# Optimization experiments

Measured on AMD Instinct MI355X. Metric: run time of the kernel, lower is better.

Reference implementation:

```python
import jax, jax.numpy as jnp
import numpy as np

N_NODES = 100000
N_EDGES = 1600000
H_IN = 128
H_OUT = 128
ELU_ALPHA = 0.1


def setup_inputs() -> dict:
    key = jax.random.key(0)
    k = jax.random.split(key, 6)
    x = jax.random.normal(k[0], (N_NODES, H_IN), dtype=jnp.float32)
    edge_index = jax.random.randint(k[1], (2, N_EDGES), 0, N_NODES, dtype=jnp.int64)
    s = 1.0 / np.sqrt(H_IN)
    W_conv = jax.random.uniform(k[2], (H_IN, H_OUT), jnp.float32, -s, s)
    b_conv = jnp.zeros((H_OUT,), jnp.float32)
    W_skip = jax.random.uniform(k[3], (H_IN, H_OUT), jnp.float32, -s, s)
    b_skip = jax.random.uniform(k[4], (H_OUT,), jnp.float32, -s, s)
    return {"x": x, "edge_index": edge_index, "W_conv": W_conv,
            "b_conv": b_conv, "W_skip": W_skip, "b_skip": b_skip}


def reference(x, edge_index, W_conv, b_conv, W_skip, b_skip):
    # GCNConv(improved=True): add self-loops with weight 2.0, symmetric norm.
    N = x.shape[0]
    src, dst = edge_index[0], edge_index[1]
    # degree = incoming edge weights (1.0 each) + 2.0 self-loop weight
    deg = jnp.zeros((N,), x.dtype).at[dst].add(1.0) + 2.0
    dinv = jax.lax.rsqrt(deg)                     # deg >= 2 always
    norm = dinv[src] * dinv[dst]                  # [E]
    h = x @ W_conv                                # [N, H_OUT]
    # scatter-add of normalized messages over real edges
    agg = jax.ops.segment_sum(norm[:, None] * h[src], dst, num_segments=N)
    # self-loop contribution: weight 2 * dinv[i]^2
    agg = agg + (2.0 * dinv * dinv)[:, None] * h
    out = agg + b_conv + x @ W_skip + b_skip
    # Dropout(p=0.1) in eval mode = identity; ELU(alpha=0.1)
    return jnp.where(out > 0, out, ELU_ALPHA * (jnp.exp(out) - 1.0))
```

## Files before the change

### kernel.cpp

```cpp
#include <hip/hip_runtime.h>
#include <hip/hip_bf16.h>
#include <hip/hip_fp16.h>

#define H 128
#define BW 128
#define BSH 7
#define NB 256

typedef __attribute__((ext_vector_type(8))) short short8;
typedef __attribute__((ext_vector_type(4))) float f32x4;

__device__ inline unsigned short f2bf(float f) {
    union { float f; unsigned int u; } v; v.f = f;
    unsigned int r = (v.u + 0x7fffu + ((v.u >> 16) & 1u)) >> 16;
    return (unsigned short)r;
}
__device__ inline float bf2f(unsigned short h) {
    union { unsigned int u; float f; } v; v.u = ((unsigned int)h) << 16;
    return v.f;
}

__global__ __launch_bounds__(256) void quant_hist_kernel(const float* __restrict__ x,
                                                         const float* __restrict__ Wc,
                                                         const float* __restrict__ Ws,
                                                         const int* __restrict__ ei,
                                                         uint* __restrict__ xq,
                                                         float* __restrict__ invs,
                                                         short8* __restrict__ wp,
                                                         int* __restrict__ counts,
                                                         int N, int E, int nbu,
                                                         int chunk, int qb) {
    __shared__ int h[1024];
    if (blockIdx.x >= qb) {
        const int b = blockIdx.x - qb;
        for (int i = threadIdx.x; i < nbu; i += 256) h[i] = 0;
        __syncthreads();
        const int lo = b * chunk;
        const int hi = min(E, lo + chunk);
        for (int e = lo + threadIdx.x; e < hi; e += 256)
            atomicAdd(&h[ei[E + e] >> BSH], 1);
        __syncthreads();
        for (int i = threadIdx.x; i < nbu; i += 256) counts[b * nbu + i] = h[i];
        return;
    }
    int node = blockIdx.x * 8 + (threadIdx.x >> 5);
    if (node < N) {
        int l32 = threadIdx.x & 31;
        float4 v = ((const float4*)x)[node * 32 + l32];
        float m = fmaxf(fmaxf(fabsf(v.x), fabsf(v.y)), fmaxf(fabsf(v.z), fabsf(v.w)));
        #pragma unroll
        for (int mk = 1; mk < 32; mk <<= 1) m = fmaxf(m, __shfl_xor(m, mk));
        m = fmaxf(m, 1e-30f);
        float s = 127.0f / m;
        int q0 = min(255, max(0, (int)rintf(v.x * s) + 128));
        int q1 = min(255, max(0, (int)rintf(v.y * s) + 128));
        int q2 = min(255, max(0, (int)rintf(v.z * s) + 128));
        int q3 = min(255, max(0, (int)rintf(v.w * s) + 128));
        xq[node * 32 + l32] = (uint)q0 | ((uint)q1 << 8) | ((uint)q2 << 16) | ((uint)q3 << 24);
        if (l32 == 0) invs[node] = m / 127.0f;
    }
    if (blockIdx.x < 8) {
        int t = blockIdx.x * 256 + threadIdx.x;
        int lane = t & 63;
        int nt = (t >> 6) & 7;
        int ks = t >> 9;
        int kbase = ks * 32 + (lane >> 4) * 8;
        int col = nt * 16 + (lane & 15);
        short8 whc, whs, wls;
        #pragma unroll
        for (int j = 0; j < 8; ++j) {
            float wc = Wc[(kbase + j) * H + col];
            float ws = Ws[(kbase + j) * H + col];
            unsigned short hc = f2bf(wc);
            unsigned short hs = f2bf(ws);
            whc[j] = (short)hc;
            whs[j] = (short)hs;
            wls[j] = (short)f2bf(ws - bf2f(hs));
        }
        int base = (ks * 8 + nt) * 64 + lane;
        wp[base] = whc;
        wp[2048 + base] = whs;
        wp[4096 + base] = wls;
    }
}

__global__ __launch_bounds__(NB) void p2_scan(const int* __restrict__ counts,
                                              int* __restrict__ scanned,
                                              int* __restrict__ btot, int nbu) {
    __shared__ int s[NB];
    const int k = blockIdx.x, t = threadIdx.x;
    int v = counts[t * nbu + k];
    s[t] = v;
    __syncthreads();
    for (int off = 1; off < NB; off <<= 1) {
        int a = (t >= off) ? s[t - off] : 0;
        __syncthreads();
        s[t] += a;
        __syncthreads();
    }
    scanned[t * nbu + k] = s[t] - v;
    if (t == NB - 1) btot[k] = s[t];
}

__global__ __launch_bounds__(256) void p5_scatter(const int* __restrict__ ei,
                                                  const int* __restrict__ btot,
                                                  const int* __restrict__ scanned,
                                                  int* __restrict__ tmp,
                                                  int* __restrict__ cstart,
                                                  int E, int nbu, int chunk) {
    __shared__ int sc[1024];
    __shared__ int part[256];
    __shared__ int lb[1024];
    const int t = threadIdx.x;
    const int b = blockIdx.x;
    const int base = t * 4;
    int v0 = (base + 0 < nbu) ? btot[base + 0] : 0;
    int v1 = (base + 1 < nbu) ? btot[base + 1] : 0;
    int v2 = (base + 2 < nbu) ? btot[base + 2] : 0;
    int v3 = (base + 3 < nbu) ? btot[base + 3] : 0;
    int s1 = v0 + v1, s2 = s1 + v2, s3 = s2 + v3;
    part[t] = s3;
    __syncthreads();
    for (int off = 1; off < 256; off <<= 1) {
        int a = (t >= off) ? part[t - off] : 0;
        __syncthreads();
        part[t] += a;
        __syncthreads();
    }
    int add = (t > 0) ? part[t - 1] : 0;
    sc[base + 0] = add;
    sc[base + 1] = add + v0;
    sc[base + 2] = add + s1;
    sc[base + 3] = add + s2;
    __syncthreads();
    if (b == 0) {
        for (int k = t; k < nbu; k += 256) cstart[k] = sc[k];
        if (t == 0) cstart[nbu] = E;
    }
    for (int k = t; k < nbu; k += 256) lb[k] = sc[k] + scanned[b * nbu + k];
    __syncthreads();
    const int lo = b * chunk;
    const int hi = min(E, lo + chunk);
    for (int e = lo + t; e < hi; e += 256) {
        int s = ei[e], d = ei[E + e];
        int slot = atomicAdd(&lb[d >> BSH], 1);
        tmp[slot] = ((d & (BW - 1)) << 17) | s;
    }
}

__global__ __launch_bounds__(256) void csra_kernel(const int* __restrict__ tmp,
                                                   const int* __restrict__ cstart,
                                                   const float* __restrict__ invs,
                                                   int* __restrict__ rstart,
                                                   float* __restrict__ dinv,
                                                   float* __restrict__ ainv,
                                                   float* __restrict__ selfw,
                                                   int N, int E) {
    __shared__ int ldeg[BW];
    __shared__ int lscan[BW];
    const int b = blockIdx.x;
    const int nstart = b << BSH;
    const int estart = cstart[b];
    const int eend = cstart[b + 1];
    const int t = threadIdx.x;

    if (t < BW) ldeg[t] = 0;
    __syncthreads();
    for (int i = estart + t; i < eend; i += 256)
        atomicAdd(&ldeg[(tmp[i] >> 17) & (BW - 1)], 1);
    __syncthreads();
    if (t < BW) lscan[t] = ldeg[t];
    __syncthreads();
    #pragma unroll
    for (int off = 1; off < BW; off <<= 1) {
        int a = 0;
        if (t < BW && t >= off) a = lscan[t - off];
        __syncthreads();
        if (t < BW) lscan[t] += a;
        __syncthreads();
    }
    if (t < BW) {
        int excl = lscan[t] - ldeg[t];
        int n = nstart + t;
        if (n < N) {
            float iv = invs[n];
            float dv = rsqrtf((float)ldeg[t] + 2.0f);
            rstart[n] = estart + excl;
            dinv[n] = dv;
            ainv[n] = dv * iv;
            selfw[n] = 2.0f * dv * dv * iv;
        }
    }
    if (b == 0 && t == 0) rstart[N] = E;
}

__global__ __launch_bounds__(256) void csrb_kernel(const int* __restrict__ tmp,
                                                   const int* __restrict__ cstart,
                                                   const int* __restrict__ rstart,
                                                   const float* __restrict__ dinv,
                                                   const float* __restrict__ ainv,
                                                   int* __restrict__ entries,
                                                   unsigned short* __restrict__ wgt,
                                                   int N, int E) {
    __shared__ int lcur[BW];
    __shared__ float ldv[BW];
    const int b = blockIdx.x;
    const int nstart = b << BSH;
    const int t = threadIdx.x;
    if (t < BW) {
        int n = nstart + t;
        lcur[t] = (n < N) ? rstart[n] : 0;
        ldv[t] = (n < N) ? dinv[n] : 0.f;
    }
    __syncthreads();
    const int estart = cstart[b];
    const int eend = cstart[b + 1];
    for (int i = estart + t; i < eend; i += 256) {
        int v = tmp[i];
        int ld = (v >> 17) & (BW - 1);
        int src = v & 0x1FFFF;
        float w = ainv[src] * ldv[ld];
        int slot = atomicAdd(&lcur[ld], 1);
        entries[slot] = src;
        wgt[slot] = __half_as_ushort(__float2half(w));
    }
}

__global__ __launch_bounds__(256) void agg_kernel(const int* __restrict__ entries,
                                                  const unsigned short* __restrict__ wgt,
                                                  const int* __restrict__ rstart,
                                                  const float* __restrict__ selfw,
                                                  const uint* __restrict__ xq,
                                                  unsigned short* __restrict__ z, int N) {
    int node = blockIdx.x * 16 + (threadIdx.x >> 4);
    if (node >= N) return;
    const int l16 = threadIdx.x & 15;
    const uint2* x2 = (const uint2*)xq;

    int start = rstart[node];
    int end = rstart[node + 1];
    float sw = selfw[node];
    uint2 qs = x2[node * 16 + l16];

    float a0 = 0.f, a1 = 0.f, a2 = 0.f, a3 = 0.f;
    float a4 = 0.f, a5 = 0.f, a6 = 0.f, a7 = 0.f;
    float sumw = 0.f;

    for (int c = start; c < end; c += 16) {
        int rem = end - c;
        int src = 0;
        float w = 0.f;
        if (l16 < rem) {
            src = entries[c + l16];
            w = __half2float(__ushort_as_half(wgt[c + l16]));
        }
        #pragma unroll 4
        for (int j = 0; j < 16; ++j) {
            int ss = __shfl(src, j, 16);
            float wv = __shfl(w, j, 16);
            if (wv != 0.f) {
                uint2 q = x2[ss * 16 + l16];
                sumw += wv;
                a0 += wv * (float)(q.x & 0xffu);
                a1 += wv * (float)((q.x >> 8) & 0xffu);
                a2 += wv * (float)((q.x >> 16) & 0xffu);
                a3 += wv * (float)(q.x >> 24);
                a4 += wv * (float)(q.y & 0xffu);
                a5 += wv * (float)((q.y >> 8) & 0xffu);
                a6 += wv * (float)((q.y >> 16) & 0xffu);
                a7 += wv * (float)(q.y >> 24);
            }
        }
    }

    sumw += sw;
    a0 += sw * (float)(qs.x & 0xffu);
    a1 += sw * (float)((qs.x >> 8) & 0xffu);
    a2 += sw * (float)((qs.x >> 16) & 0xffu);
    a3 += sw * (float)(qs.x >> 24);
    a4 += sw * (float)(qs.y & 0xffu);
    a5 += sw * (float)((qs.y >> 8) & 0xffu);
    a6 += sw * (float)((qs.y >> 16) & 0xffu);
    a7 += sw * (float)(qs.y >> 24);

    float off = 128.f * sumw;
    uint4 o;
    o.x = (uint)f2bf(a0 - off) | ((uint)f2bf(a1 - off) << 16);
    o.y = (uint)f2bf(a2 - off) | ((uint)f2bf(a3 - off) << 16);
    o.z = (uint)f2bf(a4 - off) | ((uint)f2bf(a5 - off) << 16);
    o.w = (uint)f2bf(a6 - off) | ((uint)f2bf(a7 - off) << 16);
    ((uint4*)z)[node * 16 + l16] = o;
}

__global__ __launch_bounds__(256) void gemm_kernel(const unsigned short* __restrict__ zb,
                                                   const float* __restrict__ x,
                                                   const short8* __restrict__ wp,
                                                   const float* __restrict__ bc,
                                                   const float* __restrict__ bsk,
                                                   float* __restrict__ out, int N) {
    __shared__ short8 bsm[1536];
    const int tid = threadIdx.x;
    const int lane = tid & 63;
    const int wave = tid >> 6;
    const int m = lane & 15;
    const int quad = lane >> 4;
    const int row = blockIdx.x * 64 + wave * 16 + m;
    const bool rowok = row < N;

    f32x4 acc[8];
    #pragma unroll
    for (int i = 0; i < 8; ++i) acc[i] = (f32x4){0.f, 0.f, 0.f, 0.f};

    #pragma unroll
    for (int ks = 0; ks < 4; ++ks) {
        const int k0 = ks * 32 + quad * 8;
        short8 za = {0, 0, 0, 0, 0, 0, 0, 0};
        short8 xa_h = {0, 0, 0, 0, 0, 0, 0, 0};
        short8 xa_l = {0, 0, 0, 0, 0, 0, 0, 0};
        if (rowok) {
            za = ((const short8*)zb)[(row * H + k0) >> 3];
            float4 a = *(const float4*)&x[row * H + k0];
            float4 b = *(const float4*)&x[row * H + k0 + 4];
            float xv[8] = {a.x, a.y, a.z, a.w, b.x, b.y, b.z, b.w};
            #pragma unroll
            for (int j = 0; j < 8; ++j) {
                unsigned short h = f2bf(xv[j]);
                xa_h[j] = (short)h;
                xa_l[j] = (short)f2bf(xv[j] - bf2f(h));
            }
        }
        __syncthreads();
        #pragma unroll
        for (int p = 0; p < 3; ++p) {
            bsm[p * 512 + tid]       = wp[p * 2048 + ks * 512 + tid];
            bsm[p * 512 + 256 + tid] = wp[p * 2048 + ks * 512 + 256 + tid];
        }
        __syncthreads();
        #pragma unroll
        for (int nt = 0; nt < 8; ++nt) {
            short8 bch = bsm[nt * 64 + lane];
            short8 bsh = bsm[512 + nt * 64 + lane];
            short8 bsl = bsm[1024 + nt * 64 + lane];
            acc[nt] = __builtin_amdgcn_mfma_f32_16x16x32_bf16(za, bch, acc[nt], 0, 0, 0);
            acc[nt] = __builtin_amdgcn_mfma_f32_16x16x32_bf16(xa_h, bsh, acc[nt], 0, 0, 0);
            acc[nt] = __builtin_amdgcn_mfma_f32_16x16x32_bf16(xa_l, bsh, acc[nt], 0, 0, 0);
            acc[nt] = __builtin_amdgcn_mfma_f32_16x16x32_bf16(xa_h, bsl, acc[nt], 0, 0, 0);
        }
    }

    const int orow_base = blockIdx.x * 64 + wave * 16 + quad * 4;
    #pragma unroll
    for (int nt = 0; nt < 8; ++nt) {
        int col = nt * 16 + m;
        float bias = bc[col] + bsk[col];
        #pragma unroll
        for (int r = 0; r < 4; ++r) {
            int orow = orow_base + r;
            if (orow < N) {
                float v = acc[nt][r] + bias;
                v = v > 0.f ? v : 0.1f * (__expf(v) - 1.f);
                out[orow * H + col] = v;
            }
        }
    }
}

extern "C" void kernel_launch(void* const* d_in, const int* in_sizes, int n_in,
                              void* d_out, int out_size, void* d_ws, size_t ws_size,
                              hipStream_t stream) {
    const float* x   = (const float*)d_in[0];
    const int*   ei  = (const int*)d_in[1];
    const float* Wc  = (const float*)d_in[2];
    const float* bc  = (const float*)d_in[3];
    const float* Wsk = (const float*)d_in[4];
    const float* bsk = (const float*)d_in[5];
    float* out = (float*)d_out;

    const int N = in_sizes[0] / H;
    const int E = in_sizes[1] / 2;
    const int nbu = (N + BW - 1) / BW;
    const int chunk = (E + NB - 1) / NB;
    const int qb = (N + 7) / 8;

    char* w = (char*)d_ws;
    short8*         wp      = (short8*)w;
    int*            rstart  = (int*)(w + 131072);
    float*          selfw   = (float*)(w + 589824);
    int*            entries = (int*)(w + 1048576);
    unsigned short* wgt     = (unsigned short*)(w + 7471104);
    uint*           xq      = (uint*)(w + 10747904);
    unsigned short* z       = (unsigned short*)(w + 23592960);
    float*          invs    = (float*)(w + 23592960);
    float*          dinv    = (float*)(w + 23992960);
    float*          ainv    = (float*)(w + 24392960);
    int*            cstart  = (int*)(w + 24792960);
    int*            btot    = (int*)(w + 24796160);
    int*            counts  = (int*)(w + 24799360);
    int*            scanned = (int*)(w + 25600128);
    int*            tmp     = (int*)(w + 26400896);

    quant_hist_kernel<<<qb + NB, 256, 0, stream>>>(x, Wc, Wsk, ei, xq, invs, wp,
                                                   counts, N, E, nbu, chunk, qb);

    p2_scan<<<nbu, NB, 0, stream>>>(counts, scanned, btot, nbu);
    p5_scatter<<<NB, 256, 0, stream>>>(ei, btot, scanned, tmp, cstart, E, nbu, chunk);
    csra_kernel<<<nbu, 256, 0, stream>>>(tmp, cstart, invs, rstart, dinv, ainv, selfw, N, E);
    csrb_kernel<<<nbu, 256, 0, stream>>>(tmp, cstart, rstart, dinv, ainv, entries, wgt, N, E);

    agg_kernel<<<(N + 15) / 16, 256, 0, stream>>>(entries, wgt, rstart, selfw, xq, z, N);

    gemm_kernel<<<(N + 63) / 64, 256, 0, stream>>>(z, x, wp, bc, bsk, out, N);
}
```

Before: 256.4 us.

## Build CSR with global per-node degree atomics instead of two-level bucket sort

Replaces the bucketed counting sort (per-block LDS histograms, cross-block scan, bucket scatter, then two per-bucket CSR passes) with per-node global atomic degree counts, a scan to get row starts, and one scatter pass that uses per-node global atomic cursors. This removes the intermediate tmp array and two full passes over the edges. In exchange it adds about 3.2M global atomics on random addresses plus a zero-init kernel, where the old code used LDS atomics. Edge order within each row is no longer deterministic, so fp accumulation order can vary between runs.

After: 370.7 us. +44.6%, slower.

```diff
diff --git a/kernel.cpp b/kernel.cpp
--- a/kernel.cpp
+++ b/kernel.cpp
@@ -20,27 +20,26 @@
     return v.f;
 }
 
-__global__ __launch_bounds__(256) void quant_hist_kernel(const float* __restrict__ x,
-                                                         const float* __restrict__ Wc,
-                                                         const float* __restrict__ Ws,
-                                                         const int* __restrict__ ei,
-                                                         uint* __restrict__ xq,
-                                                         float* __restrict__ invs,
-                                                         short8* __restrict__ wp,
-                                                         int* __restrict__ counts,
-                                                         int N, int E, int nbu,
-                                                         int chunk, int qb) {
-    __shared__ int h[1024];
+__global__ __launch_bounds__(256) void zero_kernel(int* __restrict__ p, int n) {
+    int i = blockIdx.x * 256 + threadIdx.x;
+    if (i < n) p[i] = 0;
+}
+
+__global__ __launch_bounds__(256) void quant_deg_kernel(const float* __restrict__ x,
+                                                        const float* __restrict__ Wc,
+                                                        const float* __restrict__ Ws,
+                                                        const int* __restrict__ ei,
+                                                        uint* __restrict__ xq,
+                                                        float* __restrict__ invs,
+                                                        short8* __restrict__ wp,
+                                                        int* __restrict__ deg,
+                                                        int N, int E, int chunk, int qb) {
     if (blockIdx.x >= qb) {
         const int b = blockIdx.x - qb;
-        for (int i = threadIdx.x; i < nbu; i += 256) h[i] = 0;
-        __syncthreads();
         const int lo = b * chunk;
         const int hi = min(E, lo + chunk);
         for (int e = lo + threadIdx.x; e < hi; e += 256)
-            atomicAdd(&h[ei[E + e] >> BSH], 1);
-        __syncthreads();
-        for (int i = threadIdx.x; i < nbu; i += 256) counts[b * nbu + i] = h[i];
+            atomicAdd(&deg[ei[E + e]], 1);
         return;
     }
     int node = blockIdx.x * 8 + (threadIdx.x >> 5);
@@ -84,35 +83,46 @@
     }
 }
 
-__global__ __launch_bounds__(NB) void p2_scan(const int* __restrict__ counts,
-                                              int* __restrict__ scanned,
-                                              int* __restrict__ btot, int nbu) {
-    __shared__ int s[NB];
-    const int k = blockIdx.x, t = threadIdx.x;
-    int v = counts[t * nbu + k];
-    s[t] = v;
+__global__ __launch_bounds__(BW) void metrics_kernel(const int* __restrict__ deg,
+                                                     const float* __restrict__ invs,
+                                                     float* __restrict__ dinv,
+                                                     float* __restrict__ ainv,
+                                                     float* __restrict__ selfw,
+                                                     int* __restrict__ lofs,
+                                                     int* __restrict__ btot, int N) {
+    __shared__ int s[BW];
+    const int b = blockIdx.x, t = threadIdx.x;
+    const int n = (b << BSH) + t;
+    int d = (n < N) ? deg[n] : 0;
+    s[t] = d;
     __syncthreads();
-    for (int off = 1; off < NB; off <<= 1) {
+    #pragma unroll
+    for (int off = 1; off < BW; off <<= 1) {
         int a = (t >= off) ? s[t - off] : 0;
         __syncthreads();
         s[t] += a;
         __syncthreads();
     }
-    scanned[t * nbu + k] = s[t] - v;
-    if (t == NB - 1) btot[k] = s[t];
-}
-
-__global__ __launch_bounds__(256) void p5_scatter(const int* __restrict__ ei,
-                                                  const int* __restrict__ btot,
-                                                  const int* __restrict__ scanned,
-                                                  int* __restrict__ tmp,
-                                                  int* __restrict__ cstart,
-                                                  int E, int nbu, int chunk) {
+    if (n < N) {
+        lofs[n] = s[t] - d;
+        float iv = invs[n];
+        float dv = rsqrtf((float)d + 2.0f);
+        dinv[n] = dv;
+        ainv[n] = dv * iv;
+        selfw[n] = 2.0f * dv * dv * iv;
+    }
+    if (t == BW - 1) btot[b] = s[t];
+}
+
+__global__ __launch_bounds__(256) void rstart_kernel(const int* __restrict__ btot,
+                                                     const int* __restrict__ lofs,
+                                                     const float* __restrict__ dinv,
+                                                     int* __restrict__ rstart,
+                                                     int2* __restrict__ pk,
+                                                     int N, int E, int nbu) {
     __shared__ int sc[1024];
     __shared__ int part[256];
-    __shared__ int lb[1024];
-    const int t = threadIdx.x;
-    const int b = blockIdx.x;
+    const int t = threadIdx.x, b = blockIdx.x;
     const int base = t * 4;
     int v0 = (base + 0 < nbu) ? btot[base + 0] : 0;
     int v1 = (base + 1 < nbu) ? btot[base + 1] : 0;
@@ -133,95 +143,33 @@
     sc[base + 2] = add + s1;
     sc[base + 3] = add + s2;
     __syncthreads();
-    if (b == 0) {
-        for (int k = t; k < nbu; k += 256) cstart[k] = sc[k];
-        if (t == 0) cstart[nbu] = E;
-    }
-    for (int k = t; k < nbu; k += 256) lb[k] = sc[k] + scanned[b * nbu + k];
-    __syncthreads();
-    const int lo = b * chunk;
+    const int cs = sc[b];
+    if (t < BW) {
+        int n = (b << BSH) + t;
+        if (n < N) {
+            int r = cs + lofs[n];
+            rstart[n] = r;
+            pk[n] = make_int2(r, __float_as_int(dinv[n]));
+        }
+    }
+    if (b == 0 && t == 0) rstart[N] = E;
+}
+
+__global__ __launch_bounds__(256) void scatter_kernel(const int* __restrict__ ei,
+                                                      const int2* __restrict__ pk,
+                                                      const float* __restrict__ ainv,
+                                                      int* __restrict__ cnt,
+                                                      int* __restrict__ entries,
+                                                      unsigned short* __restrict__ wgt,
+                                                      int E, int chunk) {
+    const int lo = blockIdx.x * chunk;
     const int hi = min(E, lo + chunk);
-    for (int e = lo + t; e < hi; e += 256) {
+    for (int e = lo + threadIdx.x; e < hi; e += 256) {
         int s = ei[e], d = ei[E + e];
-        int slot = atomicAdd(&lb[d >> BSH], 1);
-        tmp[slot] = ((d & (BW - 1)) << 17) | s;
-    }
-}
-
-__global__ __launch_bounds__(256) void csra_kernel(const int* __restrict__ tmp,
-                                                   const int* __restrict__ cstart,
-                                                   const float* __restrict__ invs,
-                                                   int* __restrict__ rstart,
-                                                   float* __restrict__ dinv,
-                                                   float* __restrict__ ainv,
-                                                   float* __restrict__ selfw,
-                                                   int N, int E) {
-    __shared__ int ldeg[BW];
-    __shared__ int lscan[BW];
-    const int b = blockIdx.x;
-    const int nstart = b << BSH;
-    const int estart = cstart[b];
-    const int eend = cstart[b + 1];
-    const int t = threadIdx.x;
-
-    if (t < BW) ldeg[t] = 0;
-    __syncthreads();
-    for (int i = estart + t; i < eend; i += 256)
-        atomicAdd(&ldeg[(tmp[i] >> 17) & (BW - 1)], 1);
-    __syncthreads();
-    if (t < BW) lscan[t] = ldeg[t];
-    __syncthreads();
-    #pragma unroll
-    for (int off = 1; off < BW; off <<= 1) {
-        int a = 0;
-        if (t < BW && t >= off) a = lscan[t - off];
-        __syncthreads();
-        if (t < BW) lscan[t] += a;
-        __syncthreads();
-    }
-    if (t < BW) {
-        int excl = lscan[t] - ldeg[t];
-        int n = nstart + t;
-        if (n < N) {
-            float iv = invs[n];
-            float dv = rsqrtf((float)ldeg[t] + 2.0f);
-            rstart[n] = estart + excl;
-            dinv[n] = dv;
-            ainv[n] = dv * iv;
-            selfw[n] = 2.0f * dv * dv * iv;
-        }
-    }
-    if (b == 0 && t == 0) rstart[N] = E;
-}
-
-__global__ __launch_bounds__(256) void csrb_kernel(const int* __restrict__ tmp,
-                                                   const int* __restrict__ cstart,
-                                                   const int* __restrict__ rstart,
-                                                   const float* __restrict__ dinv,
-                                                   const float* __restrict__ ainv,
-                                                   int* __restrict__ entries,
-                                                   unsigned short* __restrict__ wgt,
-                                                   int N, int E) {
-    __shared__ int lcur[BW];
-    __shared__ float ldv[BW];
-    const int b = blockIdx.x;
-    const int nstart = b << BSH;
-    const int t = threadIdx.x;
-    if (t < BW) {
-        int n = nstart + t;
-        lcur[t] = (n < N) ? rstart[n] : 0;
-        ldv[t] = (n < N) ? dinv[n] : 0.f;
-    }
-    __syncthreads();
-    const int estart = cstart[b];
-    const int eend = cstart[b + 1];
-    for (int i = estart + t; i < eend; i += 256) {
-        int v = tmp[i];
-        int ld = (v >> 17) & (BW - 1);
-        int src = v & 0x1FFFF;
-        float w = ainv[src] * ldv[ld];
-        int slot = atomicAdd(&lcur[ld], 1);
-        entries[slot] = src;
+        int2 p = pk[d];
+        float w = ainv[s] * __int_as_float(p.y);
+        int slot = p.x + atomicAdd(&cnt[d], 1);
+        entries[slot] = s;
         wgt[slot] = __half_as_ushort(__float2half(w));
     }
 }
@@ -393,19 +341,22 @@
     float*          invs    = (float*)(w + 23592960);
     float*          dinv    = (float*)(w + 23992960);
     float*          ainv    = (float*)(w + 24392960);
-    int*            cstart  = (int*)(w + 24792960);
-    int*            btot    = (int*)(w + 24796160);
-    int*            counts  = (int*)(w + 24799360);
-    int*            scanned = (int*)(w + 25600128);
-    int*            tmp     = (int*)(w + 26400896);
-
-    quant_hist_kernel<<<qb + NB, 256, 0, stream>>>(x, Wc, Wsk, ei, xq, invs, wp,
-                                                   counts, N, E, nbu, chunk, qb);
-
-    p2_scan<<<nbu, NB, 0, stream>>>(counts, scanned, btot, nbu);
-    p5_scatter<<<NB, 256, 0, stream>>>(ei, btot, scanned, tmp, cstart, E, nbu, chunk);
-    csra_kernel<<<nbu, 256, 0, stream>>>(tmp, cstart, invs, rstart, dinv, ainv, selfw, N, E);
-    csrb_kernel<<<nbu, 256, 0, stream>>>(tmp, cstart, rstart, dinv, ainv, entries, wgt, N, E);
+    int*            lofs    = (int*)(w + 24792960);
+    int*            btot    = (int*)(w + 25192960);
+    int*            deg     = (int*)(w + 25197056);
+    int*            cnt     = (int*)(w + 25597056);
+    int2*           pk      = (int2*)(w + 25997056);
+
+    zero_kernel<<<(2 * N + 255) / 256, 256, 0, stream>>>(deg, 2 * N);
+
+    quant_deg_kernel<<<qb + NB, 256, 0, stream>>>(x, Wc, Wsk, ei, xq, invs, wp,
+                                                  deg, N, E, chunk, qb);
+
+    metrics_kernel<<<nbu, BW, 0, stream>>>(deg, invs, dinv, ainv, selfw, lofs, btot, N);
+
+    rstart_kernel<<<nbu, 256, 0, stream>>>(btot, lofs, dinv, rstart, pk, N, E, nbu);
+
+    scatter_kernel<<<NB, 256, 0, stream>>>(ei, pk, ainv, cnt, entries, wgt, E, chunk);
 
     agg_kernel<<<(N + 15) / 16, 256, 0, stream>>>(entries, wgt, rstart, selfw, xq, z, N);
 
```

## Compute per-node degrees via global atomics in histogram pass, drop csra pass

Applied to the files above, without the earlier changes.

The histogram pass now also counts per-node in-degree with global atomics into a zeroed array. A new node_kernel derives row starts, dinv, ainv and self weights from those degrees plus the bucket totals, so the separate csra pass that re-read the bucketed edge buffer is removed. The exchange is a zeroing launch and 1.6M global atomics added to the histogram pass, against one fewer pass over the temporary edge array.

Result: slower. 333.5 us (+30.1%).

```diff
diff --git a/kernel.cpp b/kernel.cpp
--- a/kernel.cpp
+++ b/kernel.cpp
@@ -18,6 +18,11 @@
 __device__ inline float bf2f(unsigned short h) {
     union { unsigned int u; float f; } v; v.u = ((unsigned int)h) << 16;
     return v.f;
+}
+
+__global__ __launch_bounds__(256) void zero_kernel(int* __restrict__ p, int n) {
+    int i = blockIdx.x * 256 + threadIdx.x;
+    if (i < n) p[i] = 0;
 }
 
 __global__ __launch_bounds__(256) void quant_hist_kernel(const float* __restrict__ x,
@@ -28,6 +33,7 @@
                                                          float* __restrict__ invs,
                                                          short8* __restrict__ wp,
                                                          int* __restrict__ counts,
+                                                         int* __restrict__ deg,
                                                          int N, int E, int nbu,
                                                          int chunk, int qb) {
     __shared__ int h[1024];
@@ -37,8 +43,11 @@
         __syncthreads();
         const int lo = b * chunk;
         const int hi = min(E, lo + chunk);
-        for (int e = lo + threadIdx.x; e < hi; e += 256)
-            atomicAdd(&h[ei[E + e] >> BSH], 1);
+        for (int e = lo + threadIdx.x; e < hi; e += 256) {
+            int d = ei[E + e];
+            atomicAdd(&h[d >> BSH], 1);
+            atomicAdd(&deg[d], 1);
+        }
         __syncthreads();
         for (int i = threadIdx.x; i < nbu; i += 256) counts[b * nbu + i] = h[i];
         return;
@@ -100,6 +109,61 @@
     }
     scanned[t * nbu + k] = s[t] - v;
     if (t == NB - 1) btot[k] = s[t];
+}
+
+__global__ __launch_bounds__(256) void node_kernel(const int* __restrict__ deg,
+                                                   const float* __restrict__ invs,
+                                                   const int* __restrict__ btot,
+                                                   int* __restrict__ rstart,
+                                                   float* __restrict__ dinv,
+                                                   float* __restrict__ ainv,
+                                                   float* __restrict__ selfw,
+                                                   int N, int E, int nbu) {
+    __shared__ int sc[1024];
+    __shared__ int part[256];
+    __shared__ int s[BW];
+    const int t = threadIdx.x, b = blockIdx.x;
+    const int base = t * 4;
+    int v0 = (base + 0 < nbu) ? btot[base + 0] : 0;
+    int v1 = (base + 1 < nbu) ? btot[base + 1] : 0;
+    int v2 = (base + 2 < nbu) ? btot[base + 2] : 0;
+    int v3 = (base + 3 < nbu) ? btot[base + 3] : 0;
+    int s1 = v0 + v1, s2 = s1 + v2, s3 = s2 + v3;
+    part[t] = s3;
+    const int n = (b << BSH) + t;
+    int d = 0;
+    if (t < BW) { d = (n < N) ? deg[n] : 0; s[t] = d; }
+    __syncthreads();
+    for (int off = 1; off < 256; off <<= 1) {
+        int a = (t >= off) ? part[t - off] : 0;
+        __syncthreads();
+        part[t] += a;
+        __syncthreads();
+    }
+    int add = (t > 0) ? part[t - 1] : 0;
+    sc[base + 0] = add;
+    sc[base + 1] = add + v0;
+    sc[base + 2] = add + s1;
+    sc[base + 3] = add + s2;
+    #pragma unroll
+    for (int off = 1; off < BW; off <<= 1) {
+        int a = 0;
+        if (t < BW && t >= off) a = s[t - off];
+        __syncthreads();
+        if (t < BW) s[t] += a;
+        __syncthreads();
+    }
+    const int cs = sc[b];
+    if (t < BW && n < N) {
+        int excl = s[t] - d;
+        rstart[n] = cs + excl;
+        float iv = invs[n];
+        float dv = rsqrtf((float)d + 2.0f);
+        dinv[n] = dv;
+        ainv[n] = dv * iv;
+        selfw[n] = 2.0f * dv * dv * iv;
+    }
+    if (b == 0 && t == 0) rstart[N] = E;
 }
 
 __global__ __launch_bounds__(256) void p5_scatter(const int* __restrict__ ei,
@@ -148,52 +212,6 @@
     }
 }
 
-__global__ __launch_bounds__(256) void csra_kernel(const int* __restrict__ tmp,
-                                                   const int* __restrict__ cstart,
-                                                   const float* __restrict__ invs,
-                                                   int* __restrict__ rstart,
-                                                   float* __restrict__ dinv,
-                                                   float* __restrict__ ainv,
-                                                   float* __restrict__ selfw,
-                                                   int N, int E) {
-    __shared__ int ldeg[BW];
-    __shared__ int lscan[BW];
-    const int b = blockIdx.x;
-    const int nstart = b << BSH;
-    const int estart = cstart[b];
-    const int eend = cstart[b + 1];
-    const int t = threadIdx.x;
-
-    if (t < BW) ldeg[t] = 0;
-    __syncthreads();
-    for (int i = estart + t; i < eend; i += 256)
-        atomicAdd(&ldeg[(tmp[i] >> 17) & (BW - 1)], 1);
-    __syncthreads();
-    if (t < BW) lscan[t] = ldeg[t];
-    __syncthreads();
-    #pragma unroll
-    for (int off = 1; off < BW; off <<= 1) {
-        int a = 0;
-        if (t < BW && t >= off) a = lscan[t - off];
-        __syncthreads();
-        if (t < BW) lscan[t] += a;
-        __syncthreads();
-    }
-    if (t < BW) {
-        int excl = lscan[t] - ldeg[t];
-        int n = nstart + t;
-        if (n < N) {
-            float iv = invs[n];
-            float dv = rsqrtf((float)ldeg[t] + 2.0f);
-            rstart[n] = estart + excl;
-            dinv[n] = dv;
-            ainv[n] = dv * iv;
-            selfw[n] = 2.0f * dv * dv * iv;
-        }
-    }
-    if (b == 0 && t == 0) rstart[N] = E;
-}
-
 __global__ __launch_bounds__(256) void csrb_kernel(const int* __restrict__ tmp,
                                                    const int* __restrict__ cstart,
                                                    const int* __restrict__ rstart,
@@ -393,18 +411,24 @@
     float*          invs    = (float*)(w + 23592960);
     float*          dinv    = (float*)(w + 23992960);
     float*          ainv    = (float*)(w + 24392960);
-    int*            cstart  = (int*)(w + 24792960);
-    int*            btot    = (int*)(w + 24796160);
-    int*            counts  = (int*)(w + 24799360);
-    int*            scanned = (int*)(w + 25600128);
-    int*            tmp     = (int*)(w + 26400896);
+    int*            deg     = (int*)(w + 24792960);
+    int*            btot    = (int*)(w + 25192960);
+    int*            counts  = (int*)(w + 25197056);
+    int*            scanned = (int*)(w + 26001920);
+    int*            tmp     = (int*)(w + 26806784);
+    int*            cstart  = (int*)(w + 33206784);
+
+    zero_kernel<<<(N + 255) / 256, 256, 0, stream>>>(deg, N);
 
     quant_hist_kernel<<<qb + NB, 256, 0, stream>>>(x, Wc, Wsk, ei, xq, invs, wp,
-                                                   counts, N, E, nbu, chunk, qb);
+                                                   counts, deg, N, E, nbu, chunk, qb);
 
     p2_scan<<<nbu, NB, 0, stream>>>(counts, scanned, btot, nbu);
+
+    node_kernel<<<nbu, 256, 0, stream>>>(deg, invs, btot, rstart, dinv, ainv, selfw, N, E, nbu);
+
     p5_scatter<<<NB, 256, 0, stream>>>(ei, btot, scanned, tmp, cstart, E, nbu, chunk);
-    csra_kernel<<<nbu, 256, 0, stream>>>(tmp, cstart, invs, rstart, dinv, ainv, selfw, N, E);
+
     csrb_kernel<<<nbu, 256, 0, stream>>>(tmp, cstart, rstart, dinv, ainv, entries, wgt, N, E);
 
     agg_kernel<<<(N + 15) / 16, 256, 0, stream>>>(entries, wgt, rstart, selfw, xq, z, N);
```

## Fuse CSR build kernels, compute edge weights in aggregation, restructure bucket scan

Applied to the files above, without the earlier changes.

Merges the two CSR construction kernels into one, so the per-bucket local offsets feed the entry placement directly from shared memory without a second launch or a reread of tmp. The fp16 per-edge weight array is dropped, and the aggregation kernel recomputes each weight as ainv[src]*dinv[node]. That costs an extra gathered load per edge in exchange for less write traffic during CSR build. The column scan is rewritten so each block handles 32 buckets with a tiled segmented scan instead of one block per bucket running a log-step scan.

Result: faster. 251.1 us (-2.1%).

```diff
diff --git a/kernel.cpp b/kernel.cpp
--- a/kernel.cpp
+++ b/kernel.cpp
@@ -6,6 +6,7 @@
 #define BW 128
 #define BSH 7
 #define NB 256
+#define TK 32
 
 typedef __attribute__((ext_vector_type(8))) short short8;
 typedef __attribute__((ext_vector_type(4))) float f32x4;
@@ -84,22 +85,34 @@
     }
 }
 
-__global__ __launch_bounds__(NB) void p2_scan(const int* __restrict__ counts,
-                                              int* __restrict__ scanned,
-                                              int* __restrict__ btot, int nbu) {
-    __shared__ int s[NB];
-    const int k = blockIdx.x, t = threadIdx.x;
-    int v = counts[t * nbu + k];
-    s[t] = v;
-    __syncthreads();
-    for (int off = 1; off < NB; off <<= 1) {
-        int a = (t >= off) ? s[t - off] : 0;
-        __syncthreads();
-        s[t] += a;
-        __syncthreads();
-    }
-    scanned[t * nbu + k] = s[t] - v;
-    if (t == NB - 1) btot[k] = s[t];
+__global__ __launch_bounds__(256) void p2_scan(const int* __restrict__ counts,
+                                               int* __restrict__ scanned,
+                                               int* __restrict__ btot, int nbu) {
+    __shared__ int tile[NB][TK + 1];
+    __shared__ int segsum[8][TK + 1];
+    const int tl = threadIdx.x & 31;
+    const int tw = threadIdx.x >> 5;
+    const int k = blockIdx.x * TK + tl;
+    const bool kok = k < nbu;
+    for (int r = tw; r < NB; r += 8)
+        tile[r][tl] = kok ? counts[r * nbu + k] : 0;
+    __syncthreads();
+    const int base = tw * 32;
+    int s = 0;
+    #pragma unroll
+    for (int i = 0; i < 32; ++i) s += tile[base + i][tl];
+    segsum[tw][tl] = s;
+    __syncthreads();
+    int run = 0;
+    for (int q = 0; q < tw; ++q) run += segsum[q][tl];
+    if (kok) {
+        for (int i = 0; i < 32; ++i) {
+            int cur = tile[base + i][tl];
+            scanned[(base + i) * nbu + k] = run;
+            run += cur;
+        }
+        if (tw == 7) btot[k] = run;
+    }
 }
 
 __global__ __launch_bounds__(256) void p5_scatter(const int* __restrict__ ei,
@@ -148,16 +161,18 @@
     }
 }
 
-__global__ __launch_bounds__(256) void csra_kernel(const int* __restrict__ tmp,
-                                                   const int* __restrict__ cstart,
-                                                   const float* __restrict__ invs,
-                                                   int* __restrict__ rstart,
-                                                   float* __restrict__ dinv,
-                                                   float* __restrict__ ainv,
-                                                   float* __restrict__ selfw,
-                                                   int N, int E) {
+__global__ __launch_bounds__(256) void csr_kernel(const int* __restrict__ tmp,
+                                                  const int* __restrict__ cstart,
+                                                  const float* __restrict__ invs,
+                                                  int* __restrict__ entries,
+                                                  int* __restrict__ rstart,
+                                                  float* __restrict__ dinv,
+                                                  float* __restrict__ ainv,
+                                                  float* __restrict__ selfw,
+                                                  int N, int E) {
     __shared__ int ldeg[BW];
     __shared__ int lscan[BW];
+    __shared__ int lcur[BW];
     const int b = blockIdx.x;
     const int nstart = b << BSH;
     const int estart = cstart[b];
@@ -181,6 +196,7 @@
     }
     if (t < BW) {
         int excl = lscan[t] - ldeg[t];
+        lcur[t] = excl;
         int n = nstart + t;
         if (n < N) {
             float iv = invs[n];
@@ -191,44 +207,19 @@
             selfw[n] = 2.0f * dv * dv * iv;
         }
     }
-    if (b == 0 && t == 0) rstart[N] = E;
-}
-
-__global__ __launch_bounds__(256) void csrb_kernel(const int* __restrict__ tmp,
-                                                   const int* __restrict__ cstart,
-                                                   const int* __restrict__ rstart,
-                                                   const float* __restrict__ dinv,
-                                                   const float* __restrict__ ainv,
-                                                   int* __restrict__ entries,
-                                                   unsigned short* __restrict__ wgt,
-                                                   int N, int E) {
-    __shared__ int lcur[BW];
-    __shared__ float ldv[BW];
-    const int b = blockIdx.x;
-    const int nstart = b << BSH;
-    const int t = threadIdx.x;
-    if (t < BW) {
-        int n = nstart + t;
-        lcur[t] = (n < N) ? rstart[n] : 0;
-        ldv[t] = (n < N) ? dinv[n] : 0.f;
-    }
-    __syncthreads();
-    const int estart = cstart[b];
-    const int eend = cstart[b + 1];
+    __syncthreads();
     for (int i = estart + t; i < eend; i += 256) {
         int v = tmp[i];
-        int ld = (v >> 17) & (BW - 1);
-        int src = v & 0x1FFFF;
-        float w = ainv[src] * ldv[ld];
-        int slot = atomicAdd(&lcur[ld], 1);
-        entries[slot] = src;
-        wgt[slot] = __half_as_ushort(__float2half(w));
-    }
+        int sl = atomicAdd(&lcur[(v >> 17) & (BW - 1)], 1);
+        entries[estart + sl] = v & 0x1FFFF;
+    }
+    if (b == 0 && t == 0) rstart[N] = E;
 }
 
 __global__ __launch_bounds__(256) void agg_kernel(const int* __restrict__ entries,
-                                                  const unsigned short* __restrict__ wgt,
                                                   const int* __restrict__ rstart,
+                                                  const float* __restrict__ dinv,
+                                                  const float* __restrict__ ainv,
                                                   const float* __restrict__ selfw,
                                                   const uint* __restrict__ xq,
                                                   unsigned short* __restrict__ z, int N) {
@@ -239,6 +230,7 @@
 
     int start = rstart[node];
     int end = rstart[node + 1];
+    float dd = dinv[node];
     float sw = selfw[node];
     uint2 qs = x2[node * 16 + l16];
 
@@ -252,7 +244,7 @@
         float w = 0.f;
         if (l16 < rem) {
             src = entries[c + l16];
-            w = __half2float(__ushort_as_half(wgt[c + l16]));
+            w = ainv[src] * dd;
         }
         #pragma unroll 4
         for (int j = 0; j < 16; ++j) {
@@ -385,29 +377,31 @@
     char* w = (char*)d_ws;
     short8*         wp      = (short8*)w;
     int*            rstart  = (int*)(w + 131072);
-    float*          selfw   = (float*)(w + 589824);
-    int*            entries = (int*)(w + 1048576);
-    unsigned short* wgt     = (unsigned short*)(w + 7471104);
-    uint*           xq      = (uint*)(w + 10747904);
-    unsigned short* z       = (unsigned short*)(w + 23592960);
-    float*          invs    = (float*)(w + 23592960);
-    float*          dinv    = (float*)(w + 23992960);
-    float*          ainv    = (float*)(w + 24392960);
-    int*            cstart  = (int*)(w + 24792960);
-    int*            btot    = (int*)(w + 24796160);
-    int*            counts  = (int*)(w + 24799360);
-    int*            scanned = (int*)(w + 25600128);
-    int*            tmp     = (int*)(w + 26400896);
+    float*          dinv    = (float*)(w + 540672);
+    float*          ainv    = (float*)(w + 942080);
+    float*          selfw   = (float*)(w + 1343488);
+    int*            entries = (int*)(w + 1744896);
+    uint*           xq      = (uint*)(w + 8146944);
+    unsigned short* z       = (unsigned short*)(w + 20971520);
+    float*          invs    = (float*)(w + 20971520);
+    int*            cstart  = (int*)(w + 21371520);
+    int*            btot    = (int*)(w + 21374784);
+    int*            counts  = (int*)(w + 21377984);
+    int*            scanned = (int*)(w + 22178752);
+    int*            tmp     = (int*)(w + 22979520);
 
     quant_hist_kernel<<<qb + NB, 256, 0, stream>>>(x, Wc, Wsk, ei, xq, invs, wp,
                                                    counts, N, E, nbu, chunk, qb);
 
-    p2_scan<<<nbu, NB, 0, stream>>>(counts, scanned, btot, nbu);
+    p2_scan<<<(nbu + TK - 1) / TK, 256, 0, stream>>>(counts, scanned, btot, nbu);
+
     p5_scatter<<<NB, 256, 0, stream>>>(ei, btot, scanned, tmp, cstart, E, nbu, chunk);
-    csra_kernel<<<nbu, 256, 0, stream>>>(tmp, cstart, invs, rstart, dinv, ainv, selfw, N, E);
-    csrb_kernel<<<nbu, 256, 0, stream>>>(tmp, cstart, rstart, dinv, ainv, entries, wgt, N, E);
-
-    agg_kernel<<<(N + 15) / 16, 256, 0, stream>>>(entries, wgt, rstart, selfw, xq, z, N);
+
+    csr_kernel<<<nbu, 256, 0, stream>>>(tmp, cstart, invs, entries, rstart,
+                                        dinv, ainv, selfw, N, E);
+
+    agg_kernel<<<(N + 15) / 16, 256, 0, stream>>>(entries, rstart, dinv, ainv,
+                                                  selfw, xq, z, N);
 
     gemm_kernel<<<(N + 63) / 64, 256, 0, stream>>>(z, x, wp, bc, bsk, out, N);
 }
```
